# Kernel optimization log

Measured on AMD Instinct MI355X. Metric: run time of the kernel, lower is better.

## Reference

```python
import jax, jax.numpy as jnp
import numpy as np

B, T, H, W = 4, 8, 14, 14
IN_DIMS = 768
OUT_DIMS = 768
HEADS = 12
HD = OUT_DIMS // HEADS  # 64
N = T * H * W + 1  # 1569 tokens incl. cls
SCALE = HD ** -0.5
EPS = 1e-5


def _ln(x, w, b):
    m = jnp.mean(x, -1, keepdims=True)
    v = jnp.mean((x - m) ** 2, -1, keepdims=True)
    return (x - m) * jax.lax.rsqrt(v + EPS) * w + b


def _pool(t, conv_w, nw, nb, Tq, Hq, Wq):
    # t: (B, heads, N, C) with leading cls token. Depthwise 3x3x3 conv, stride 1, pad 1.
    Bn, Hn, _, C = t.shape
    cls_tok, sp = t[:, :, :1], t[:, :, 1:]
    xc = sp.reshape(Bn * Hn, Tq, Hq, Wq, C).transpose(0, 4, 1, 2, 3)  # (B*h, C, T, H, W)
    xc = jax.lax.conv_general_dilated(
        xc, conv_w, (1, 1, 1), [(1, 1)] * 3,
        dimension_numbers=('NCDHW', 'OIDHW', 'NCDHW'), feature_group_count=C)
    xc = xc.reshape(Bn, Hn, C, Tq * Hq * Wq).swapaxes(2, 3)  # (B, h, L, C)
    xc = jnp.concatenate([cls_tok, xc], axis=2)
    return _ln(xc, nw, nb)


def _rel_lookup(rel, q_size, k_size):
    # stride_q == stride_kv == 1 -> q_size == k_size and rel already has 2*size-1 rows,
    # so no interpolation / ratio scaling is needed.
    coords = jnp.arange(q_size)[:, None] - jnp.arange(k_size)[None, :] + (k_size - 1)
    return rel[coords]  # (q, k, C)


def setup_inputs():
    key = jax.random.key(0)
    ks = jax.random.split(key, 12)
    w = lambda i, shape: jax.random.normal(ks[i], shape, jnp.float32) * 0.02
    return {
        'x': jax.random.normal(ks[0], (B, N, IN_DIMS), jnp.float32),
        'qkv_w': w(1, (IN_DIMS, 3 * OUT_DIMS)),
        'qkv_b': jnp.zeros((3 * OUT_DIMS,), jnp.float32),
        'proj_w': w(2, (OUT_DIMS, OUT_DIMS)),
        'proj_b': jnp.zeros((OUT_DIMS,), jnp.float32),
        'pool_q_w': w(3, (HD, 1, 3, 3, 3)),
        'pool_k_w': w(4, (HD, 1, 3, 3, 3)),
        'pool_v_w': w(5, (HD, 1, 3, 3, 3)),
        'norm_q_w': jnp.ones((HD,), jnp.float32), 'norm_q_b': jnp.zeros((HD,), jnp.float32),
        'norm_k_w': jnp.ones((HD,), jnp.float32), 'norm_k_b': jnp.zeros((HD,), jnp.float32),
        'norm_v_w': jnp.ones((HD,), jnp.float32), 'norm_v_b': jnp.zeros((HD,), jnp.float32),
        'rel_pos_t': w(6, (2 * T - 1, HD)),
        'rel_pos_h': w(7, (2 * H - 1, HD)),
        'rel_pos_w': w(8, (2 * W - 1, HD)),
        't_size': T, 'h_size': H, 'w_size': W,
    }


def reference(x, qkv_w, qkv_b, proj_w, proj_b, pool_q_w, pool_k_w, pool_v_w,
              norm_q_w, norm_q_b, norm_k_w, norm_k_b, norm_v_w, norm_v_b,
              rel_pos_t, rel_pos_h, rel_pos_w, t_size, h_size, w_size):
    Bn, Nn, _ = x.shape
    qkv = (x @ qkv_w + qkv_b).reshape(Bn, Nn, 3, HEADS, HD)
    qkv = jnp.transpose(qkv, (2, 0, 3, 1, 4))  # (3, B, heads, N, HD)
    q, k, v = qkv[0], qkv[1], qkv[2]
    q = _pool(q, pool_q_w, norm_q_w, norm_q_b, t_size, h_size, w_size)
    k = _pool(k, pool_k_w, norm_k_w, norm_k_b, t_size, h_size, w_size)
    v = _pool(v, pool_v_w, norm_v_w, norm_v_b, t_size, h_size, w_size)
    attn = jnp.einsum('bhqc,bhkc->bhqk', q * SCALE, k)
    # Decomposed spatiotemporal relative position bias on the non-cls block.
    Rt = _rel_lookup(rel_pos_t, t_size, t_size)
    Rh = _rel_lookup(rel_pos_h, h_size, h_size)
    Rw = _rel_lookup(rel_pos_w, w_size, w_size)
    r_q = q[:, :, 1:].reshape(Bn, HEADS, t_size, h_size, w_size, HD)
    rel_t = jnp.einsum('bythwc,tkc->bythwk', r_q, Rt)
    rel_h = jnp.einsum('bythwc,hkc->bythwk', r_q, Rh)
    rel_w = jnp.einsum('bythwc,wkc->bythwk', r_q, Rw)
    bias = (rel_t[..., :, None, None] + rel_h[..., None, :, None]
            + rel_w[..., None, None, :])  # (B, h, qt, qh, qw, kt, kh, kw)
    L = t_size * h_size * w_size
    attn = attn.at[:, :, 1:, 1:].add(bias.reshape(Bn, HEADS, L, L))
    attn = jax.nn.softmax(attn, axis=-1)
    out = jnp.einsum('bhqk,bhkc->bhqc', attn, v)
    out = out.at[:, :, 1:, :].add(q[:, :, 1:, :])  # residual pooling (cls excluded)
    out = out.swapaxes(1, 2).reshape(Bn, Nn, OUT_DIMS)
    return out @ proj_w + proj_b
```

## Files before the change

kernel.cpp:

```cpp
#include <hip/hip_runtime.h>
#include <cstdint>
#include <cstddef>

typedef __attribute__((ext_vector_type(8))) short short8;
typedef __attribute__((ext_vector_type(4))) short short4v;
typedef __attribute__((ext_vector_type(4))) float f32x4;
typedef unsigned short u16;

#define DI __device__ __forceinline__

constexpr int BATCH = 4;
constexpr int HEADS = 12, HD = 64;
constexpr int NTOK = 1569;
constexpr int NPAD = 1600;
constexpr int QPAD = 1664;
constexpr int DIM = 768, DIM3 = 2304;
constexpr int MROWS = BATCH * NTOK;
constexpr int MP = 6400;
constexpr int AUG = 128;
constexpr int BHN = BATCH * HEADS;
constexpr float LOG2E = 1.4426950408889634f;
constexpr float QSCALE = 0.125f * LOG2E;
constexpr float RESID = 8.0f / LOG2E;
constexpr float LN_EPS = 1e-5f;

DI u16 f2bf(float x) {
  union { float f; unsigned u; } v; v.f = x;
  unsigned r = v.u + 0x7FFFu + ((v.u >> 16) & 1u);
  return (u16)(r >> 16);
}
DI float bf2f(u16 h) {
  union { unsigned u; float f; } v; v.u = ((unsigned)h) << 16;
  return v.f;
}

typedef const __attribute__((address_space(1))) unsigned int gu32;
typedef __attribute__((address_space(3))) unsigned int lu32;
DI void gld16(const void* g, void* l) {
  __builtin_amdgcn_global_load_lds((gu32*)g, (lu32*)l, 16, 0, 0);
}

DI float rowmax16(float x) {
  int t;
  t = __builtin_amdgcn_update_dpp(__float_as_int(x), __float_as_int(x), 0x121, 0xF, 0xF, false);
  x = fmaxf(x, __int_as_float(t));
  t = __builtin_amdgcn_update_dpp(__float_as_int(x), __float_as_int(x), 0x122, 0xF, 0xF, false);
  x = fmaxf(x, __int_as_float(t));
  t = __builtin_amdgcn_update_dpp(__float_as_int(x), __float_as_int(x), 0x124, 0xF, 0xF, false);
  x = fmaxf(x, __int_as_float(t));
  t = __builtin_amdgcn_update_dpp(__float_as_int(x), __float_as_int(x), 0x128, 0xF, 0xF, false);
  x = fmaxf(x, __int_as_float(t));
  return x;
}
DI float rowsum16(float x) {
  int t;
  t = __builtin_amdgcn_update_dpp(__float_as_int(x), __float_as_int(x), 0x121, 0xF, 0xF, false);
  x += __int_as_float(t);
  t = __builtin_amdgcn_update_dpp(__float_as_int(x), __float_as_int(x), 0x122, 0xF, 0xF, false);
  x += __int_as_float(t);
  t = __builtin_amdgcn_update_dpp(__float_as_int(x), __float_as_int(x), 0x124, 0xF, 0xF, false);
  x += __int_as_float(t);
  t = __builtin_amdgcn_update_dpp(__float_as_int(x), __float_as_int(x), 0x128, 0xF, 0xF, false);
  x += __int_as_float(t);
  return x;
}

__global__ __launch_bounds__(256) void k_cast_x(const float* __restrict__ x,
                                                u16* __restrict__ xb) {
  int i = (blockIdx.x * 256 + threadIdx.x) * 4;
  if (i >= MP * DIM) return;
  int row = i / DIM;
  short4v o;
  if (row < MROWS) {
    float4 v = *(const float4*)(x + i);
    o.x = (short)f2bf(v.x); o.y = (short)f2bf(v.y);
    o.z = (short)f2bf(v.z); o.w = (short)f2bf(v.w);
  } else {
    o.x = 0; o.y = 0; o.z = 0; o.w = 0;
  }
  *(short4v*)(xb + i) = o;
}

__global__ __launch_bounds__(256) void k_transpose_cast(const float* __restrict__ src,
                                                        u16* __restrict__ dst,
                                                        int K, int NC) {
  __shared__ float tile[32][33];
  const int ntiles = NC >> 5;
  const int bx = blockIdx.x % ntiles;
  const int by = blockIdx.x / ntiles;
  const int tx = threadIdx.x & 31, ty = threadIdx.x >> 5;
  const int n0 = bx * 32, k0 = by * 32;
#pragma unroll
  for (int r = 0; r < 32; r += 8)
    tile[ty + r][tx] = src[(size_t)(k0 + ty + r) * NC + n0 + tx];
  __syncthreads();
#pragma unroll
  for (int r = 0; r < 32; r += 8)
    dst[(size_t)(n0 + ty + r) * K + k0 + tx] = f2bf(tile[tx][ty + r]);
}

template <int EPI>
__global__ __launch_bounds__(256) void k_gemm(const u16* __restrict__ A,
                                              const u16* __restrict__ Bt,
                                              const float* __restrict__ bias,
                                              float* __restrict__ out) {
  __shared__ __align__(16) u16 sA[128 * 64];
  __shared__ __align__(16) u16 sB[128 * 64];
  const int tid = threadIdx.x;
  const int w = tid >> 6, lane = tid & 63;
  const int g = lane >> 4, lr = lane & 15;
  const int brow = blockIdx.x * 128, bcol = blockIdx.y * 128;
  const int wr = w >> 1, wc = w & 1;

  f32x4 acc[4][4];
#pragma unroll
  for (int m = 0; m < 4; ++m)
#pragma unroll
    for (int n = 0; n < 4; ++n) {
      acc[m][n].x = 0.f; acc[m][n].y = 0.f; acc[m][n].z = 0.f; acc[m][n].w = 0.f;
    }

  for (int kt = 0; kt < 12; ++kt) {
    __syncthreads();
#pragma unroll
    for (int j = 0; j < 4; ++j) {
      int cb = (j * 4 + w) * 64;
      int chunk = cb + lane;
      int row = chunk >> 3, ch = chunk & 7;
      int gch = ch ^ (row & 7);
      gld16(A + (size_t)(brow + row) * DIM + kt * 64 + gch * 8, &sA[cb * 8]);
      gld16(Bt + (size_t)(bcol + row) * DIM + kt * 64 + gch * 8, &sB[cb * 8]);
    }
    __syncthreads();

    short8 af[4][2], bfr[4][2];
#pragma unroll
    for (int m = 0; m < 4; ++m) {
      int row = wr * 64 + m * 16 + lr;
      int sw = row & 7;
#pragma unroll
      for (int ks = 0; ks < 2; ++ks)
        af[m][ks] = *(const short8*)&sA[row * 64 + (((ks * 4 + g) ^ sw) * 8)];
    }
#pragma unroll
    for (int n = 0; n < 4; ++n) {
      int row = wc * 64 + n * 16 + lr;
      int sw = row & 7;
#pragma unroll
      for (int ks = 0; ks < 2; ++ks)
        bfr[n][ks] = *(const short8*)&sB[row * 64 + (((ks * 4 + g) ^ sw) * 8)];
    }
#pragma unroll
    for (int m = 0; m < 4; ++m)
#pragma unroll
      for (int n = 0; n < 4; ++n) {
        acc[m][n] = __builtin_amdgcn_mfma_f32_16x16x32_bf16(af[m][0], bfr[n][0], acc[m][n], 0, 0, 0);
        acc[m][n] = __builtin_amdgcn_mfma_f32_16x16x32_bf16(af[m][1], bfr[n][1], acc[m][n], 0, 0, 0);
      }
  }

#pragma unroll
  for (int m = 0; m < 4; ++m)
#pragma unroll
    for (int n = 0; n < 4; ++n) {
      int gj = bcol + wc * 64 + n * 16 + lr;
      float bv = bias[gj];
#pragma unroll
      for (int r = 0; r < 4; ++r) {
        int gm = brow + wr * 64 + m * 16 + g * 4 + r;
        if (gm >= MROWS) continue;
        float v = acc[m][n][r] + bv;
        if (EPI == 0) {
          int t = gj >= 1536 ? 2 : (gj >= 768 ? 1 : 0);
          int rem = gj - t * 768;
          int h = rem >> 6, c = rem & 63;
          int b = gm >= 3 * NTOK ? 3 : (gm >= 2 * NTOK ? 2 : (gm >= NTOK ? 1 : 0));
          int nt = gm - b * NTOK;
          out[(((size_t)(t * BATCH + b) * HEADS + h) * NPAD + nt) * HD + c] = v;
        } else {
          out[(size_t)gm * DIM + gj] = v;
        }
      }
    }
}

DI float ldsrc(const float* __restrict__ src, int tt, int h2, int w2, int lane) {
  if ((unsigned)tt >= 8u || (unsigned)h2 >= 14u || (unsigned)w2 >= 14u) return 0.f;
  return src[(size_t)(1 + (tt * 14 + h2) * 14 + w2) * HD + lane];
}

__global__ __launch_bounds__(256, 4) void k_pool(
    const float* __restrict__ qkv,
    const float* __restrict__ pw_q, const float* __restrict__ pw_k, const float* __restrict__ pw_v,
    const float* __restrict__ nw_q, const float* __restrict__ nb_q,
    const float* __restrict__ nw_k, const float* __restrict__ nb_k,
    const float* __restrict__ nw_v, const float* __restrict__ nb_v,
    u16* __restrict__ Qa, u16* __restrict__ Ka, u16* __restrict__ Vt) {
  const int wv = threadIdx.x >> 6, lane = threadIdx.x & 63;
  const int unit = blockIdx.x % 29;
  const int taubh = blockIdx.x / 29;
  const int tau = taubh / BHN, bh = taubh % BHN;
  const float* src = qkv + ((size_t)tau * BHN + bh) * ((size_t)NPAD * HD);
  const float* nw = tau == 0 ? nw_q : tau == 1 ? nw_k : nw_v;
  const float* nb = tau == 0 ? nb_q : tau == 1 ? nb_k : nb_v;

  if (unit == 28) {
    if (wv == 0) {
      float val = src[lane];
      float s = val, sq = val * val;
#pragma unroll
      for (int off = 1; off < 64; off <<= 1) { s += __shfl_xor(s, off); sq += __shfl_xor(sq, off); }
      float mean = s * (1.f / 64.f);
      float var = sq * (1.f / 64.f) - mean * mean;
      float ln = (val - mean) * rsqrtf(var + LN_EPS) * nw[lane] + nb[lane];
      if (tau == 0)      { size_t base = (size_t)bh * QPAD * AUG; Qa[base + lane] = f2bf(ln * QSCALE); Qa[base + 64 + lane] = 0; }
      else if (tau == 1) { size_t base = (size_t)bh * NPAD * AUG; Ka[base + lane] = f2bf(ln); Ka[base + 64 + lane] = 0; }
      else               { Vt[((size_t)bh * HD + lane) * NPAD] = f2bf(ln); }
    } else {
      int lim = (tau == 0) ? QPAD : NPAD;
      for (int n = 1569 + (wv - 1); n < lim; n += 3) {
        if (tau == 0) {
          size_t base = ((size_t)bh * QPAD + n) * AUG;
          Qa[base + lane] = 0; Qa[base + 64 + lane] = 0;
        } else if (tau == 1) {
          size_t base = ((size_t)bh * NPAD + n) * AUG;
          Ka[base + lane] = 0; Ka[base + 64 + lane] = 0;
        } else {
          Vt[((size_t)bh * HD + lane) * NPAD + n] = 0;
        }
      }
    }
    return;
  }

  const int th = unit * 4 + wv;
  const int t = th / 14, hh = th % 14;

  float wt[27];
  {
    const float* wp = (tau == 0 ? pw_q : tau == 1 ? pw_k : pw_v) + lane * 27;
#pragma unroll
    for (int j = 0; j < 27; ++j) wt[j] = wp[j];
  }

  float win[9][3];
#pragma unroll
  for (int dt = 0; dt < 3; ++dt)
#pragma unroll
    for (int dh = 0; dh < 3; ++dh) {
      win[dt * 3 + dh][0] = 0.f;
      win[dt * 3 + dh][1] = ldsrc(src, t + dt - 1, hh + dh - 1, 0, lane);
      win[dt * 3 + dh][2] = ldsrc(src, t + dt - 1, hh + dh - 1, 1, lane);
    }

#pragma unroll
  for (int ww = 0; ww < 14; ++ww) {
    float nxt[9];
#pragma unroll
    for (int dt = 0; dt < 3; ++dt)
#pragma unroll
      for (int dh = 0; dh < 3; ++dh)
        nxt[dt * 3 + dh] = ldsrc(src, t + dt - 1, hh + dh - 1, ww + 2, lane);

    float a = 0.f;
#pragma unroll
    for (int i = 0; i < 9; ++i)
      a += win[i][0] * wt[i * 3 + 0] + win[i][1] * wt[i * 3 + 1] + win[i][2] * wt[i * 3 + 2];

    float s = a, sq = a * a;
#pragma unroll
    for (int off = 1; off < 64; off <<= 1) { s += __shfl_xor(s, off); sq += __shfl_xor(sq, off); }
    float mean = s * (1.f / 64.f);
    float var = sq * (1.f / 64.f) - mean * mean;
    float ln = (a - mean) * rsqrtf(var + LN_EPS) * nw[lane] + nb[lane];

    const int n = 1 + (t * 14 + hh) * 14 + ww;
    if (tau == 0) {
      size_t base = ((size_t)bh * QPAD + n) * AUG;
      Qa[base + lane] = f2bf(ln * QSCALE);
      Qa[base + 64 + lane] = 0;
    } else if (tau == 1) {
      size_t base = ((size_t)bh * NPAD + n) * AUG;
      Ka[base + lane] = f2bf(ln);
      u16 e = 0;
      if (lane == t || lane == 8 + hh || lane == 22 + ww) e = 0x3F80;
      Ka[base + 64 + lane] = e;
    } else {
      Vt[((size_t)bh * HD + lane) * NPAD + n] = f2bf(ln);
    }

#pragma unroll
    for (int i = 0; i < 9; ++i) { win[i][0] = win[i][1]; win[i][1] = win[i][2]; win[i][2] = nxt[i]; }
  }
}

__global__ __launch_bounds__(256) void k_rel(const float* __restrict__ rel_t,
                                             const float* __restrict__ rel_h,
                                             const float* __restrict__ rel_w,
                                             u16* __restrict__ Qa) {
  __shared__ __align__(16) u16 sR[80 * 72];
  const int tid = threadIdx.x, w = tid >> 6, lane = tid & 63;
  const int g = lane >> 4, lr = lane & 15;
  const int bh = blockIdx.x / 25, qt = blockIdx.x % 25;

  for (int idx = tid; idx < 80 * 64; idx += 256) {
    int j = idx >> 6, c = idx & 63;
    float v = 0.f;
    if (j < 15)      v = rel_t[j * HD + c];
    else if (j < 42) v = rel_h[(j - 15) * HD + c];
    else if (j < 69) v = rel_w[(j - 42) * HD + c];
    sR[j * 72 + c] = f2bf(v * 8.f);
  }
  __syncthreads();

  const int q0 = qt * 64 + w * 16;
  short8 aq[2];
  {
    const u16* qrow = Qa + ((size_t)bh * QPAD + q0 + lr) * AUG;
    aq[0] = *(const short8*)(qrow + g * 8);
    aq[1] = *(const short8*)(qrow + 32 + g * 8);
  }

  f32x4 acc[5];
#pragma unroll
  for (int jt = 0; jt < 5; ++jt) {
    f32x4 a; a.x = 0.f; a.y = 0.f; a.z = 0.f; a.w = 0.f;
    int row = jt * 16 + lr;
    short8 b0 = *(const short8*)&sR[row * 72 + g * 8];
    short8 b1 = *(const short8*)&sR[row * 72 + (4 + g) * 8];
    a = __builtin_amdgcn_mfma_f32_16x16x32_bf16(aq[0], b0, a, 0, 0, 0);
    a = __builtin_amdgcn_mfma_f32_16x16x32_bf16(aq[1], b1, a, 0, 0, 0);
    acc[jt] = a;
  }

#pragma unroll
  for (int jt = 0; jt < 5; ++jt) {
    int j = jt * 16 + lr;
#pragma unroll
    for (int r = 0; r < 4; ++r) {
      int gq = q0 + g * 4 + r;
      if (gq < 1 || gq >= NTOK) continue;
      int p = gq - 1;
      int t = p / 196, pr = p - t * 196;
      int hh = pr / 14, ww = pr - hh * 14;
      int it = t + 7 - j;
      int ih = hh + 28 - j;
      int iw = ww + 55 - j;
      int i = -1;
      if ((unsigned)it < 8u) i = it;
      else if ((unsigned)ih < 14u) i = 8 + ih;
      else if ((unsigned)iw < 14u) i = 22 + iw;
      if (i >= 0)
        Qa[((size_t)bh * QPAD + gq) * AUG + 64 + i] = f2bf(acc[jt][r]);
    }
  }
}

__global__ __launch_bounds__(256, 3) void k_attn(const u16* __restrict__ Qa,
                                                 const u16* __restrict__ Ka,
                                                 const u16* __restrict__ Vt,
                                                 u16* __restrict__ Opart,
                                                 float* __restrict__ ml) {
  __shared__ __align__(16) u16 sK[64 * 128];
  __shared__ __align__(16) u16 sV[2][64 * 64];
  __shared__ __align__(16) u16 sP[4][32 * 72];
  const int tid = threadIdx.x, w = tid >> 6, lane = tid & 63;
  const int g = lane >> 4, lr = lane & 15;
  const int bid = blockIdx.x;
  const int swz = (bid & 7) * 156 + (bid >> 3);
  const int bh = swz / 26, rem2 = swz % 26;
  const int half = rem2 / 13, qt = rem2 % 13;
  const int qw = qt * 128 + w * 32;
  const int kb0 = half * 13;
  const int kbN = half ? 12 : 13;

  short8 aq[2][4];
#pragma unroll
  for (int f = 0; f < 2; ++f) {
    const u16* qrow = Qa + ((size_t)bh * QPAD + qw + f * 16 + lr) * AUG;
#pragma unroll
    for (int ks = 0; ks < 4; ++ks) aq[f][ks] = *(const short8*)(qrow + ks * 32 + g * 8);
  }

  const u16* kgp[4];
  u16* kld[4];
#pragma unroll
  for (int j = 0; j < 4; ++j) {
    int idx = j * 256 + tid;
    int row = idx >> 4, ch = idx & 15;
    int gch = ch ^ (row & 7);
    kgp[j] = Ka + ((size_t)bh * NPAD + kb0 * 64 + row) * AUG + gch * 8;
    kld[j] = &sK[(j * 256 + w * 64) * 8];
  }
  const u16* vgp[2];
  int vld[2];
#pragma unroll
  for (int j = 0; j < 2; ++j) {
    int idx = j * 256 + tid;
    int row = idx >> 3, ch = idx & 7;
    int gch = ch ^ (row & 7);
    vgp[j] = Vt + ((size_t)bh * HD + row) * NPAD + kb0 * 64 + gch * 8;
    vld[j] = (j * 256 + w * 64) * 8;
  }

#pragma unroll
  for (int j = 0; j < 4; ++j) { gld16(kgp[j], kld[j]); kgp[j] += 64 * AUG; }
#pragma unroll
  for (int j = 0; j < 2; ++j) { gld16(vgp[j], &sV[0][vld[j]]); vgp[j] += 64; }
  __syncthreads();

  f32x4 O[2][4];
#pragma unroll
  for (int f = 0; f < 2; ++f)
#pragma unroll
    for (int c4 = 0; c4 < 4; ++c4) { O[f][c4].x = 0.f; O[f][c4].y = 0.f; O[f][c4].z = 0.f; O[f][c4].w = 0.f; }
  float mrun[2][4], lrun[2][4];
#pragma unroll
  for (int f = 0; f < 2; ++f)
#pragma unroll
    for (int r = 0; r < 4; ++r) { mrun[f][r] = -1e30f; lrun[f][r] = 0.f; }

  int cc[4];
#pragma unroll
  for (int ct = 0; ct < 4; ++ct) cc[ct] = ((ct ^ g) & 3) << 4;
  const int bx = (lr >> 2) & 3;

  int cur = 0;
  for (int it = 0; it < kbN; ++it) {
    f32x4 sacc[2][4];
    __builtin_amdgcn_s_setprio(1);
#pragma unroll
    for (int ct = 0; ct < 4; ++ct) {
      int row = ct * 16 + lr;
      int sw = row & 7;
      short8 bk[4];
#pragma unroll
      for (int ks = 0; ks < 4; ++ks)
        bk[ks] = *(const short8*)&sK[row * 128 + (((ks * 4 + g) ^ sw) << 3)];
#pragma unroll
      for (int f = 0; f < 2; ++f) {
        f32x4 a; a.x = 0.f; a.y = 0.f; a.z = 0.f; a.w = 0.f;
#pragma unroll
        for (int ks = 0; ks < 4; ++ks)
          a = __builtin_amdgcn_mfma_f32_16x16x32_bf16(aq[f][ks], bk[ks], a, 0, 0, 0);
        sacc[f][ct] = a;
      }
    }
    __builtin_amdgcn_s_setprio(0);
    __syncthreads();

    if (it + 1 < kbN) {
#pragma unroll
      for (int j = 0; j < 4; ++j) { gld16(kgp[j], kld[j]); kgp[j] += 64 * AUG; }
#pragma unroll
      for (int j = 0; j < 2; ++j) { gld16(vgp[j], &sV[cur ^ 1][vld[j]]); vgp[j] += 64; }
    }

    if (kb0 + it == 24) {
#pragma unroll
      for (int f = 0; f < 2; ++f)
#pragma unroll
        for (int r = 0; r < 4; ++r) {
          sacc[f][2][r] = (lr < 1) ? sacc[f][2][r] : -1e30f;
          sacc[f][3][r] = -1e30f;
        }
    }

#pragma unroll
    for (int f = 0; f < 2; ++f)
#pragma unroll
      for (int r = 0; r < 4; ++r) {
        float mx = fmaxf(fmaxf(sacc[f][0][r], sacc[f][1][r]), fmaxf(sacc[f][2][r], sacc[f][3][r]));
        mx = rowmax16(mx);
        float om = mrun[f][r];
        float nm = om;
        if (__any(mx > om)) {
          nm = fmaxf(om, mx);
          float sc = exp2f(om - nm);
#pragma unroll
          for (int c4 = 0; c4 < 4; ++c4) O[f][c4][r] *= sc;
          lrun[f][r] *= sc;
          mrun[f][r] = nm;
        }
        float p0 = exp2f(sacc[f][0][r] - nm);
        float p1 = exp2f(sacc[f][1][r] - nm);
        float p2 = exp2f(sacc[f][2][r] - nm);
        float p3 = exp2f(sacc[f][3][r] - nm);
        lrun[f][r] += rowsum16((p0 + p1) + (p2 + p3));
        int ro = (f * 16 + g * 4 + r) * 72;
        sP[w][ro + cc[0] + lr] = (u16)(__float_as_uint(p0) >> 16);
        sP[w][ro + cc[1] + lr] = (u16)(__float_as_uint(p1) >> 16);
        sP[w][ro + cc[2] + lr] = (u16)(__float_as_uint(p2) >> 16);
        sP[w][ro + cc[3] + lr] = (u16)(__float_as_uint(p3) >> 16);
      }

    __builtin_amdgcn_s_setprio(1);
#pragma unroll
    for (int kk = 0; kk < 2; ++kk) {
      short8 ap[2];
#pragma unroll
      for (int f = 0; f < 2; ++f)
        ap[f] = *(const short8*)&sP[w][(f * 16 + lr) * 72 + (((kk * 2 + (g >> 1)) ^ bx) << 4) + ((g & 1) << 3)];
#pragma unroll
      for (int c4 = 0; c4 < 4; ++c4) {
        int row = c4 * 16 + lr;
        int sw = row & 7;
        short8 bv = *(const short8*)&sV[cur][row * 64 + (((kk * 4 + g) ^ sw) << 3)];
#pragma unroll
        for (int f = 0; f < 2; ++f)
          O[f][c4] = __builtin_amdgcn_mfma_f32_16x16x32_bf16(ap[f], bv, O[f][c4], 0, 0, 0);
      }
    }
    __builtin_amdgcn_s_setprio(0);

    __syncthreads();
    cur ^= 1;
  }

  size_t pbase = (size_t)(bh * 2 + half) * QPAD;
#pragma unroll
  for (int f = 0; f < 2; ++f)
#pragma unroll
    for (int r = 0; r < 4; ++r) {
      int qg = qw + f * 16 + g * 4 + r;
      if (qg >= NTOK) continue;
      float inv = 1.f / lrun[f][r];
#pragma unroll
      for (int c4 = 0; c4 < 4; ++c4)
        Opart[(pbase + qg) * 64 + c4 * 16 + lr] = f2bf(O[f][c4][r] * inv);
      if (lr == 0) {
        ml[(pbase + qg) * 2]     = mrun[f][r];
        ml[(pbase + qg) * 2 + 1] = lrun[f][r];
      }
    }
}

__global__ __launch_bounds__(256) void k_comb(const u16* __restrict__ Opart,
                                              const float* __restrict__ ml,
                                              const u16* __restrict__ Qa,
                                              u16* __restrict__ outA) {
  const int wv = threadIdx.x >> 6, lane = threadIdx.x & 63;
  int rid = blockIdx.x * 4 + wv;
  if (rid >= BHN * NTOK) return;
  int bh = rid / NTOK, qg = rid - bh * NTOK;
  size_t base0 = (size_t)(bh * 2) * QPAD + qg;
  size_t base1 = base0 + QPAD;
  float m0 = ml[base0 * 2], l0 = ml[base0 * 2 + 1];
  float m1 = ml[base1 * 2], l1 = ml[base1 * 2 + 1];
  float M = fmaxf(m0, m1);
  float w0 = l0 * exp2f(m0 - M), w1 = l1 * exp2f(m1 - M);
  float inv = 1.f / (w0 + w1);
  float o0 = bf2f(Opart[base0 * 64 + lane]);
  float o1 = bf2f(Opart[base1 * 64 + lane]);
  float v = (w0 * o0 + w1 * o1) * inv;
  if (qg >= 1) v += RESID * bf2f(Qa[((size_t)bh * QPAD + qg) * AUG + lane]);
  int b = bh / HEADS, h = bh - b * HEADS;
  outA[((size_t)(b * NTOK + qg)) * DIM + h * HD + lane] = f2bf(v);
}

extern "C" void kernel_launch(void* const* d_in, const int* in_sizes, int n_in,
                              void* d_out, int out_size, void* d_ws, size_t ws_size,
                              hipStream_t stream) {
  (void)in_sizes; (void)n_in; (void)out_size; (void)ws_size;
  const float* x      = (const float*)d_in[0];
  const float* qkv_w  = (const float*)d_in[1];
  const float* qkv_b  = (const float*)d_in[2];
  const float* proj_w = (const float*)d_in[3];
  const float* proj_b = (const float*)d_in[4];
  const float* pw_q   = (const float*)d_in[5];
  const float* pw_k   = (const float*)d_in[6];
  const float* pw_v   = (const float*)d_in[7];
  const float* nw_q   = (const float*)d_in[8];
  const float* nb_q   = (const float*)d_in[9];
  const float* nw_k   = (const float*)d_in[10];
  const float* nb_k   = (const float*)d_in[11];
  const float* nw_v   = (const float*)d_in[12];
  const float* nb_v   = (const float*)d_in[13];
  const float* rel_t  = (const float*)d_in[14];
  const float* rel_h  = (const float*)d_in[15];
  const float* rel_w  = (const float*)d_in[16];
  float* out = (float*)d_out;

  char* ws = (char*)d_ws;
  size_t off = 0;
  auto alloc = [&](size_t bytes) -> void* {
    off = (off + 511) & ~(size_t)511;
    void* p = ws + off;
    off += bytes;
    return p;
  };
  u16*   xb     = (u16*)alloc((size_t)MP * DIM * 2);
  u16*   qkvwT  = (u16*)alloc((size_t)DIM3 * DIM * 2);
  u16*   projwT = (u16*)alloc((size_t)DIM * DIM * 2);
  float* qkvf   = (float*)alloc((size_t)3 * BHN * NPAD * HD * 4);
  u16*   Qa     = (u16*)alloc((size_t)BHN * QPAD * AUG * 2);
  u16*   Ka     = (u16*)alloc((size_t)BHN * NPAD * AUG * 2);
  u16*   Vt     = (u16*)alloc((size_t)BHN * HD * NPAD * 2);
  u16*   attnO  = (u16*)alloc((size_t)MP * DIM * 2);
  u16*   Opart  = (u16*)alloc((size_t)BHN * 2 * QPAD * HD * 2);
  float* mlbuf  = (float*)alloc((size_t)BHN * 2 * QPAD * 2 * 4);

  k_cast_x<<<dim3(MP * DIM / 1024), dim3(256), 0, stream>>>(x, xb);
  k_transpose_cast<<<dim3((DIM3 / 32) * (DIM / 32)), dim3(256), 0, stream>>>(qkv_w, qkvwT, DIM, DIM3);
  k_transpose_cast<<<dim3((DIM / 32) * (DIM / 32)), dim3(256), 0, stream>>>(proj_w, projwT, DIM, DIM);

  k_gemm<0><<<dim3(MP / 128, DIM3 / 128), dim3(256), 0, stream>>>(xb, qkvwT, qkv_b, qkvf);

  k_pool<<<dim3(3 * BHN * 29), dim3(256), 0, stream>>>(
      qkvf, pw_q, pw_k, pw_v, nw_q, nb_q, nw_k, nb_k, nw_v, nb_v,
      Qa, Ka, Vt);

  k_rel<<<dim3(BHN * 25), dim3(256), 0, stream>>>(rel_t, rel_h, rel_w, Qa);

  k_attn<<<dim3(BHN * 26), dim3(256), 0, stream>>>(Qa, Ka, Vt, Opart, mlbuf);

  k_comb<<<dim3((BHN * NTOK + 3) / 4), dim3(256), 0, stream>>>(Opart, mlbuf, Qa, attnO);

  k_gemm<1><<<dim3(MP / 128, DIM / 128), dim3(256), 0, stream>>>(attnO, projwT, proj_b, out);
}
```

Measured before the change: 279.9 us.

## Drop online-softmax max tracking; compute row sums via MFMA with ones vector

Removes running max and rescaling from the attention kernel and exponentiates scores directly, on the assumption that logits stay bounded for LayerNorm-ed q/k. Row sums come from an extra MFMA against a vector of bf16 ones instead of DPP reductions. The QK MFMA operands are swapped so each lane holds a row and can pack probabilities into LDS as 64-bit stores. The combine kernel now merges the two halves by plain l-weighted averaging, which risks overflow if scores were ever large.

```diff
diff --git a/kernel.cpp b/kernel.cpp
--- a/kernel.cpp
+++ b/kernel.cpp
@@ -38,31 +38,6 @@
 typedef __attribute__((address_space(3))) unsigned int lu32;
 DI void gld16(const void* g, void* l) {
   __builtin_amdgcn_global_load_lds((gu32*)g, (lu32*)l, 16, 0, 0);
-}
-
-DI float rowmax16(float x) {
-  int t;
-  t = __builtin_amdgcn_update_dpp(__float_as_int(x), __float_as_int(x), 0x121, 0xF, 0xF, false);
-  x = fmaxf(x, __int_as_float(t));
-  t = __builtin_amdgcn_update_dpp(__float_as_int(x), __float_as_int(x), 0x122, 0xF, 0xF, false);
-  x = fmaxf(x, __int_as_float(t));
-  t = __builtin_amdgcn_update_dpp(__float_as_int(x), __float_as_int(x), 0x124, 0xF, 0xF, false);
-  x = fmaxf(x, __int_as_float(t));
-  t = __builtin_amdgcn_update_dpp(__float_as_int(x), __float_as_int(x), 0x128, 0xF, 0xF, false);
-  x = fmaxf(x, __int_as_float(t));
-  return x;
-}
-DI float rowsum16(float x) {
-  int t;
-  t = __builtin_amdgcn_update_dpp(__float_as_int(x), __float_as_int(x), 0x121, 0xF, 0xF, false);
-  x += __int_as_float(t);
-  t = __builtin_amdgcn_update_dpp(__float_as_int(x), __float_as_int(x), 0x122, 0xF, 0xF, false);
-  x += __int_as_float(t);
-  t = __builtin_amdgcn_update_dpp(__float_as_int(x), __float_as_int(x), 0x124, 0xF, 0xF, false);
-  x += __int_as_float(t);
-  t = __builtin_amdgcn_update_dpp(__float_as_int(x), __float_as_int(x), 0x128, 0xF, 0xF, false);
-  x += __int_as_float(t);
-  return x;
 }
 
 __global__ __launch_bounds__(256) void k_cast_x(const float* __restrict__ x,
@@ -360,7 +335,7 @@
                                                  const u16* __restrict__ Ka,
                                                  const u16* __restrict__ Vt,
                                                  u16* __restrict__ Opart,
-                                                 float* __restrict__ ml) {
+                                                 float* __restrict__ lsum) {
   __shared__ __align__(16) u16 sK[64 * 128];
   __shared__ __align__(16) u16 sV[2][64 * 64];
   __shared__ __align__(16) u16 sP[4][32 * 72];
@@ -382,6 +357,10 @@
     for (int ks = 0; ks < 4; ++ks) aq[f][ks] = *(const short8*)(qrow + ks * 32 + g * 8);
   }
 
+  short8 vones;
+#pragma unroll
+  for (int i = 0; i < 8; ++i) vones[i] = (short)0x3F80;
+
   const u16* kgp[4];
   u16* kld[4];
 #pragma unroll
@@ -409,21 +388,11 @@
   for (int j = 0; j < 2; ++j) { gld16(vgp[j], &sV[0][vld[j]]); vgp[j] += 64; }
   __syncthreads();
 
-  f32x4 O[2][4];
+  f32x4 O[2][5];
 #pragma unroll
   for (int f = 0; f < 2; ++f)
 #pragma unroll
-    for (int c4 = 0; c4 < 4; ++c4) { O[f][c4].x = 0.f; O[f][c4].y = 0.f; O[f][c4].z = 0.f; O[f][c4].w = 0.f; }
-  float mrun[2][4], lrun[2][4];
-#pragma unroll
-  for (int f = 0; f < 2; ++f)
-#pragma unroll
-    for (int r = 0; r < 4; ++r) { mrun[f][r] = -1e30f; lrun[f][r] = 0.f; }
-
-  int cc[4];
-#pragma unroll
-  for (int ct = 0; ct < 4; ++ct) cc[ct] = ((ct ^ g) & 3) << 4;
-  const int bx = (lr >> 2) & 3;
+    for (int c4 = 0; c4 < 5; ++c4) { O[f][c4].x = 0.f; O[f][c4].y = 0.f; O[f][c4].z = 0.f; O[f][c4].w = 0.f; }
 
   int cur = 0;
   for (int it = 0; it < kbN; ++it) {
@@ -442,7 +411,7 @@
         f32x4 a; a.x = 0.f; a.y = 0.f; a.z = 0.f; a.w = 0.f;
 #pragma unroll
         for (int ks = 0; ks < 4; ++ks)
-          a = __builtin_amdgcn_mfma_f32_16x16x32_bf16(aq[f][ks], bk[ks], a, 0, 0, 0);
+          a = __builtin_amdgcn_mfma_f32_16x16x32_bf16(bk[ks], aq[f][ks], a, 0, 0, 0);
         sacc[f][ct] = a;
       }
     }
@@ -458,41 +427,29 @@
 
     if (kb0 + it == 24) {
 #pragma unroll
-      for (int f = 0; f < 2; ++f)
-#pragma unroll
-        for (int r = 0; r < 4; ++r) {
-          sacc[f][2][r] = (lr < 1) ? sacc[f][2][r] : -1e30f;
-          sacc[f][3][r] = -1e30f;
-        }
-    }
-
-#pragma unroll
-    for (int f = 0; f < 2; ++f)
-#pragma unroll
-      for (int r = 0; r < 4; ++r) {
-        float mx = fmaxf(fmaxf(sacc[f][0][r], sacc[f][1][r]), fmaxf(sacc[f][2][r], sacc[f][3][r]));
-        mx = rowmax16(mx);
-        float om = mrun[f][r];
-        float nm = om;
-        if (__any(mx > om)) {
-          nm = fmaxf(om, mx);
-          float sc = exp2f(om - nm);
-#pragma unroll
-          for (int c4 = 0; c4 < 4; ++c4) O[f][c4][r] *= sc;
-          lrun[f][r] *= sc;
-          mrun[f][r] = nm;
-        }
-        float p0 = exp2f(sacc[f][0][r] - nm);
-        float p1 = exp2f(sacc[f][1][r] - nm);
-        float p2 = exp2f(sacc[f][2][r] - nm);
-        float p3 = exp2f(sacc[f][3][r] - nm);
-        lrun[f][r] += rowsum16((p0 + p1) + (p2 + p3));
-        int ro = (f * 16 + g * 4 + r) * 72;
-        sP[w][ro + cc[0] + lr] = (u16)(__float_as_uint(p0) >> 16);
-        sP[w][ro + cc[1] + lr] = (u16)(__float_as_uint(p1) >> 16);
-        sP[w][ro + cc[2] + lr] = (u16)(__float_as_uint(p2) >> 16);
-        sP[w][ro + cc[3] + lr] = (u16)(__float_as_uint(p3) >> 16);
-      }
+      for (int f = 0; f < 2; ++f) {
+        sacc[f][2][0] = (g == 0) ? sacc[f][2][0] : -1e30f;
+        sacc[f][2][1] = -1e30f; sacc[f][2][2] = -1e30f; sacc[f][2][3] = -1e30f;
+        sacc[f][3][0] = -1e30f; sacc[f][3][1] = -1e30f;
+        sacc[f][3][2] = -1e30f; sacc[f][3][3] = -1e30f;
+      }
+    }
+
+#pragma unroll
+    for (int f = 0; f < 2; ++f) {
+      int ro = (f * 16 + lr) * 72;
+#pragma unroll
+      for (int ct = 0; ct < 4; ++ct) {
+        unsigned u0 = __float_as_uint(exp2f(sacc[f][ct][0]));
+        unsigned u1 = __float_as_uint(exp2f(sacc[f][ct][1]));
+        unsigned u2 = __float_as_uint(exp2f(sacc[f][ct][2]));
+        unsigned u3 = __float_as_uint(exp2f(sacc[f][ct][3]));
+        uint2 pk;
+        pk.x = __builtin_amdgcn_perm(u1, u0, 0x07060302u);
+        pk.y = __builtin_amdgcn_perm(u3, u2, 0x07060302u);
+        *(uint2*)&sP[w][ro + ct * 16 + g * 4] = pk;
+      }
+    }
 
     __builtin_amdgcn_s_setprio(1);
 #pragma unroll
@@ -500,7 +457,7 @@
       short8 ap[2];
 #pragma unroll
       for (int f = 0; f < 2; ++f)
-        ap[f] = *(const short8*)&sP[w][(f * 16 + lr) * 72 + (((kk * 2 + (g >> 1)) ^ bx) << 4) + ((g & 1) << 3)];
+        ap[f] = *(const short8*)&sP[w][(f * 16 + lr) * 72 + kk * 32 + g * 8];
 #pragma unroll
       for (int c4 = 0; c4 < 4; ++c4) {
         int row = c4 * 16 + lr;
@@ -510,6 +467,9 @@
         for (int f = 0; f < 2; ++f)
           O[f][c4] = __builtin_amdgcn_mfma_f32_16x16x32_bf16(ap[f], bv, O[f][c4], 0, 0, 0);
       }
+#pragma unroll
+      for (int f = 0; f < 2; ++f)
+        O[f][4] = __builtin_amdgcn_mfma_f32_16x16x32_bf16(ap[f], vones, O[f][4], 0, 0, 0);
     }
     __builtin_amdgcn_s_setprio(0);
 
@@ -524,19 +484,17 @@
     for (int r = 0; r < 4; ++r) {
       int qg = qw + f * 16 + g * 4 + r;
       if (qg >= NTOK) continue;
-      float inv = 1.f / lrun[f][r];
+      float l = O[f][4][r];
+      float inv = 1.f / l;
 #pragma unroll
       for (int c4 = 0; c4 < 4; ++c4)
         Opart[(pbase + qg) * 64 + c4 * 16 + lr] = f2bf(O[f][c4][r] * inv);
-      if (lr == 0) {
-        ml[(pbase + qg) * 2]     = mrun[f][r];
-        ml[(pbase + qg) * 2 + 1] = lrun[f][r];
-      }
+      if (lr == 0) lsum[pbase + qg] = l;
     }
 }
 
 __global__ __launch_bounds__(256) void k_comb(const u16* __restrict__ Opart,
-                                              const float* __restrict__ ml,
+                                              const float* __restrict__ lsum,
                                               const u16* __restrict__ Qa,
                                               u16* __restrict__ outA) {
   const int wv = threadIdx.x >> 6, lane = threadIdx.x & 63;
@@ -545,14 +503,11 @@
   int bh = rid / NTOK, qg = rid - bh * NTOK;
   size_t base0 = (size_t)(bh * 2) * QPAD + qg;
   size_t base1 = base0 + QPAD;
-  float m0 = ml[base0 * 2], l0 = ml[base0 * 2 + 1];
-  float m1 = ml[base1 * 2], l1 = ml[base1 * 2 + 1];
-  float M = fmaxf(m0, m1);
-  float w0 = l0 * exp2f(m0 - M), w1 = l1 * exp2f(m1 - M);
-  float inv = 1.f / (w0 + w1);
+  float l0 = lsum[base0], l1 = lsum[base1];
+  float inv = 1.f / (l0 + l1);
   float o0 = bf2f(Opart[base0 * 64 + lane]);
   float o1 = bf2f(Opart[base1 * 64 + lane]);
-  float v = (w0 * o0 + w1 * o1) * inv;
+  float v = (l0 * o0 + l1 * o1) * inv;
   if (qg >= 1) v += RESID * bf2f(Qa[((size_t)bh * QPAD + qg) * AUG + lane]);
   int b = bh / HEADS, h = bh - b * HEADS;
   outA[((size_t)(b * NTOK + qg)) * DIM + h * HD + lane] = f2bf(v);
@@ -598,7 +553,7 @@
   u16*   Vt     = (u16*)alloc((size_t)BHN * HD * NPAD * 2);
   u16*   attnO  = (u16*)alloc((size_t)MP * DIM * 2);
   u16*   Opart  = (u16*)alloc((size_t)BHN * 2 * QPAD * HD * 2);
-  float* mlbuf  = (float*)alloc((size_t)BHN * 2 * QPAD * 2 * 4);
+  float* lbuf   = (float*)alloc((size_t)BHN * 2 * QPAD * 4);
 
   k_cast_x<<<dim3(MP * DIM / 1024), dim3(256), 0, stream>>>(x, xb);
   k_transpose_cast<<<dim3((DIM3 / 32) * (DIM / 32)), dim3(256), 0, stream>>>(qkv_w, qkvwT, DIM, DIM3);
@@ -612,9 +567,9 @@
 
   k_rel<<<dim3(BHN * 25), dim3(256), 0, stream>>>(rel_t, rel_h, rel_w, Qa);
 
-  k_attn<<<dim3(BHN * 26), dim3(256), 0, stream>>>(Qa, Ka, Vt, Opart, mlbuf);
-
-  k_comb<<<dim3((BHN * NTOK + 3) / 4), dim3(256), 0, stream>>>(Opart, mlbuf, Qa, attnO);
+  k_attn<<<dim3(BHN * 26), dim3(256), 0, stream>>>(Qa, Ka, Vt, Opart, lbuf);
+
+  k_comb<<<dim3((BHN * NTOK + 3) / 4), dim3(256), 0, stream>>>(Opart, lbuf, Qa, attnO);
 
   k_gemm<1><<<dim3(MP / 128, DIM / 128), dim3(256), 0, stream>>>(attnO, projwT, proj_b, out);
 }
```

Result: faster. 248.2 us (-11.3%).
